# Kernel tuning notes

Measured on AMD Instinct MI355X. Metric: run time of the kernel, lower is better.

The kernel has to match this reference:

```python
import jax, jax.numpy as jnp
import numpy as np

D_MODEL = 2048
N_HEADS = 16
DIM_K = 128
DIM_V = 128
D_MID = 6144
STD = 0.02


def setup_inputs() -> dict:
    key = jax.random.key(0)
    k_x, k_wq, k_wo, k_K, k_V = jax.random.split(key, 5)
    B, T = 2, 2048
    x = jax.random.normal(k_x, (B, T, D_MODEL), dtype=jnp.float32)
    # nn.Linear weights: stored as (out, in); we keep jax convention (in, out)
    Wq = jax.random.normal(k_wq, (D_MODEL, N_HEADS * DIM_K), dtype=jnp.float32) * (1.0 / np.sqrt(D_MODEL))
    Wo = jax.random.normal(k_wo, (N_HEADS * DIM_V, D_MODEL), dtype=jnp.float32) * (1.0 / np.sqrt(N_HEADS * DIM_V))
    K = jax.random.normal(k_K, (N_HEADS, D_MID, DIM_K), dtype=jnp.float32) * STD
    V = jax.random.normal(k_V, (N_HEADS, D_MID, DIM_V), dtype=jnp.float32) * STD
    return {"x": x, "Wq": Wq, "Wo": Wo, "K": K, "V": V}


def reference(x, Wq, Wo, K, V):
    B, T, _ = x.shape
    # Q projection: (b,t,d) @ (d, h*dk) -> (b,t,h,dk)
    Q = (x @ Wq).reshape(B, T, N_HEADS, DIM_K)
    # per-head GEMM 1: (b,t,h,dk) x (h,m,dk) -> (b,t,h,m)
    scores = jnp.einsum('bthk,hmk->bthm', Q, K)
    scores = jax.nn.silu(scores)
    # per-head GEMM 2: (b,t,h,m) x (h,m,dv) -> (b,t,h,dv)
    out = jnp.einsum('bthm,hmv->bthv', scores, V)
    out = out.reshape(B, T, N_HEADS * DIM_V)
    return out @ Wo
```

## Files before the change

kernel.cpp:

```cpp
#include <hip/hip_runtime.h>

typedef unsigned short ushort_t;
typedef __attribute__((ext_vector_type(8))) short bf16x8;
typedef __attribute__((ext_vector_type(4))) float f32x4;
typedef __attribute__((ext_vector_type(4))) unsigned int u32x4;

__device__ __forceinline__ unsigned short f2b(float f) {
  unsigned u = __builtin_bit_cast(unsigned, f);
  u += 0x7fffu + ((u >> 16) & 1u);
  return (unsigned short)(u >> 16);
}

__device__ __forceinline__ float silu_f(float x) {
  float e = __builtin_amdgcn_exp2f(x * -1.44269504f);
  return x * __builtin_amdgcn_rcpf(1.0f + e);
}

__device__ __forceinline__ void silu_pack(const f32x4 s, unsigned& p0, unsigned& p1) {
  float v0 = silu_f(s[0]), v1 = silu_f(s[1]), v2 = silu_f(s[2]), v3 = silu_f(s[3]);
  asm("v_cvt_pk_bf16_f32 %0, %1, %2" : "=v"(p0) : "v"(v0), "v"(v1));
  asm("v_cvt_pk_bf16_f32 %0, %1, %2" : "=v"(p1) : "v"(v2), "v"(v3));
}

__device__ __forceinline__ void gload_lds16(const ushort_t* g, ushort_t* l) {
  auto* gp = (const __attribute__((address_space(1))) ushort_t*)g;
  auto* lp = (__attribute__((address_space(3))) ushort_t*)l;
  __builtin_amdgcn_global_load_lds(gp, lp, 16, 0, 0);
}

__device__ __forceinline__ void storeC(float* C, size_t i, float v) { C[i] = v; }
__device__ __forceinline__ void storeC(ushort_t* C, size_t i, float v) { C[i] = f2b(v); }


__global__ __launch_bounds__(256) void cast_f32_bf16_k(const float4* __restrict__ in,
                                                       ushort4* __restrict__ out, int n4) {
  int i = blockIdx.x * 256 + threadIdx.x;
  if (i < n4) {
    float4 v = in[i];
    ushort4 o;
    o.x = f2b(v.x); o.y = f2b(v.y); o.z = f2b(v.z); o.w = f2b(v.w);
    out[i] = o;
  }
}

__global__ __launch_bounds__(256) void transpose_cast_k(const float* __restrict__ in,
                                                        ushort_t* __restrict__ out,
                                                        int rows, int cols) {
  __shared__ float tile[64][65];
  size_t boff = (size_t)blockIdx.z * rows * cols;
  const float* inb = in + boff;
  ushort_t* outb = out + boff;
  int r0 = blockIdx.y * 64, c0 = blockIdx.x * 64;
  int lr = threadIdx.x >> 6, lc = threadIdx.x & 63;
#pragma unroll
  for (int i = 0; i < 16; i++) {
    int r = i * 4 + lr;
    tile[r][lc] = inb[(size_t)(r0 + r) * cols + (c0 + lc)];
  }
  __syncthreads();
#pragma unroll
  for (int i = 0; i < 16; i++) {
    int oc = i * 4 + lr;
    outb[(size_t)(c0 + oc) * rows + (r0 + lc)] = f2b(tile[lc][oc]);
  }
}


template <typename OutT>
__global__ __launch_bounds__(256) void gemm_bt_k(const ushort_t* __restrict__ A,
                                                 const ushort_t* __restrict__ BT,
                                                 OutT* __restrict__ C, int M, int N, int K) {
  __shared__ alignas(16) ushort_t lA[2][128 * 32];
  __shared__ alignas(16) ushort_t lB[2][128 * 32];
  int tid = threadIdx.x, lane = tid & 63, wave = tid >> 6;
  int wm = wave >> 1, wn = wave & 1;
  int m0 = blockIdx.y * 128, n0 = blockIdx.x * 128;
  int lr = lane & 15, lk = lane >> 4;
  f32x4 acc[4][4] = {};

#define STG(B, K0)                                                                   \
  {                                                                                  \
    _Pragma("unroll") for (int t = 0; t < 2; t++) {                                  \
      int cb = wave * 128 + t * 64;                                                  \
      int c = cb + lane;                                                             \
      int r = c >> 2;                                                                \
      int kc = (c & 3) ^ ((r >> 1) & 3);                                             \
      gload_lds16(A + (size_t)(m0 + r) * K + (K0) + kc * 8, lA[B] + (size_t)cb * 8); \
      gload_lds16(BT + (size_t)(n0 + r) * K + (K0) + kc * 8, lB[B] + (size_t)cb * 8);\
    }                                                                                \
  }

  STG(0, 0);
  int cur = 0;
  for (int k0 = 0; k0 < K; k0 += 32, cur ^= 1) {
    asm volatile("s_waitcnt vmcnt(0)" ::: "memory");
    __builtin_amdgcn_s_barrier();
    asm volatile("" ::: "memory");
    if (k0 + 32 < K) STG(cur ^ 1, k0 + 32);
    bf16x8 aF[4], bF[4];
#pragma unroll
    for (int i = 0; i < 4; i++) {
      int r = wm * 64 + i * 16 + lr;
      int kc = lk ^ ((r >> 1) & 3);
      aF[i] = *(const bf16x8*)(lA[cur] + r * 32 + kc * 8);
    }
#pragma unroll
    for (int j = 0; j < 4; j++) {
      int r = wn * 64 + j * 16 + lr;
      int kc = lk ^ ((r >> 1) & 3);
      bF[j] = *(const bf16x8*)(lB[cur] + r * 32 + kc * 8);
    }
#pragma unroll
    for (int i = 0; i < 4; i++)
#pragma unroll
      for (int j = 0; j < 4; j++)
        acc[i][j] = __builtin_amdgcn_mfma_f32_16x16x32_bf16(aF[i], bF[j], acc[i][j], 0, 0, 0);
  }
#undef STG
#pragma unroll
  for (int i = 0; i < 4; i++) {
#pragma unroll
    for (int j = 0; j < 4; j++) {
      int row = m0 + wm * 64 + i * 16 + lk * 4;
      int col = n0 + wn * 64 + j * 16 + lr;
#pragma unroll
      for (int r = 0; r < 4; r++) storeC(C, (size_t)(row + r) * N + col, acc[i][j][r]);
    }
  }
}


#define MFMA_BF16 __builtin_amdgcn_mfma_f32_16x16x32_bf16

__global__ __launch_bounds__(256) void fused_mid_k(const ushort_t* __restrict__ Qb,
                                                   const ushort_t* __restrict__ Kb,
                                                   const ushort_t* __restrict__ VTb,
                                                   ushort_t* __restrict__ mid) {
  __shared__ alignas(16) ushort_t lK[2][64 * 128];
  __shared__ alignas(16) ushort_t lV[2][128 * 64];
  int tid = threadIdx.x, lane = tid & 63, wave = tid >> 6;
  int lr = lane & 15, lk = lane >> 4;
  int id = blockIdx.x;
  int h = (id & 7) * 2 + (id >> 8);
  int t0 = ((id >> 3) & 31) * 128;
  const ushort_t* Qh = Qb + (size_t)t0 * 2048 + h * 128;
  const ushort_t* Kh = Kb + (size_t)h * 6144 * 128;
  const ushort_t* Vh = VTb + (size_t)h * 128 * 6144;

  bf16x8 qF[2][4];
#pragma unroll
  for (int tj = 0; tj < 2; tj++)
#pragma unroll
    for (int ks = 0; ks < 4; ks++)
      qF[tj][ks] = *(const bf16x8*)(Qh + (size_t)(wave * 32 + tj * 16 + lr) * 2048 + ks * 32 + lk * 8);

#define STAGE(B, M0)                                                              \
  {                                                                               \
    _Pragma("unroll") for (int t = 0; t < 4; t++) {                               \
      int c = (wave * 4 + t) * 64 + lane;                                         \
      int ik = c >> 4;                                                            \
      int pik = (ik & 0x20) | ((ik & 0x0C) << 1) | ((ik & 0x10) >> 2) | (ik & 3); \
      int sk = (c & 15) ^ (ik & 15);                                              \
      gload_lds16(Kh + (size_t)((M0) + pik) * 128 + sk * 8, lK[B] + (size_t)c * 8); \
      int iv = c >> 3;                                                            \
      int sv = (c & 7) ^ (iv & 7);                                                \
      gload_lds16(Vh + (size_t)iv * 6144 + (M0) + sv * 8, lV[B] + (size_t)c * 8); \
    }                                                                             \
  }

  STAGE(0, 0);

  f32x4 acc[2][8] = {};
  int cur = 0;
  for (int m0 = 0; m0 < 6144; m0 += 64, cur ^= 1) {
    asm volatile("s_waitcnt vmcnt(0)" ::: "memory");
    __builtin_amdgcn_s_barrier();
    asm volatile("" ::: "memory");
    if (m0 + 64 < 6144) STAGE(cur ^ 1, m0 + 64);

    __builtin_amdgcn_s_setprio(1);
    f32x4 s2[4][2] = {};
    unsigned P[4][2][2];
#pragma unroll
    for (int ks = 0; ks < 4; ks++) {
      bf16x8 k0 = *(const bf16x8*)(lK[cur] + (0 * 16 + lr) * 128 + (((ks * 4 + lk) ^ lr) * 8));
      bf16x8 k1 = *(const bf16x8*)(lK[cur] + (1 * 16 + lr) * 128 + (((ks * 4 + lk) ^ lr) * 8));
      s2[0][0] = MFMA_BF16(k0, qF[0][ks], s2[0][0], 0, 0, 0);
      s2[0][1] = MFMA_BF16(k0, qF[1][ks], s2[0][1], 0, 0, 0);
      s2[1][0] = MFMA_BF16(k1, qF[0][ks], s2[1][0], 0, 0, 0);
      s2[1][1] = MFMA_BF16(k1, qF[1][ks], s2[1][1], 0, 0, 0);
    }
#pragma unroll
    for (int ks = 0; ks < 4; ks++) {
      bf16x8 k2 = *(const bf16x8*)(lK[cur] + (2 * 16 + lr) * 128 + (((ks * 4 + lk) ^ lr) * 8));
      bf16x8 k3 = *(const bf16x8*)(lK[cur] + (3 * 16 + lr) * 128 + (((ks * 4 + lk) ^ lr) * 8));
      s2[2][0] = MFMA_BF16(k2, qF[0][ks], s2[2][0], 0, 0, 0);
      s2[2][1] = MFMA_BF16(k2, qF[1][ks], s2[2][1], 0, 0, 0);
      s2[3][0] = MFMA_BF16(k3, qF[0][ks], s2[3][0], 0, 0, 0);
      s2[3][1] = MFMA_BF16(k3, qF[1][ks], s2[3][1], 0, 0, 0);
      {
        int mj = ks >> 1, tjj = ks & 1;
        silu_pack(s2[mj][tjj], P[mj][tjj][0], P[mj][tjj][1]);
      }
    }
    bf16x8 aF0[2];
#pragma unroll
    for (int tj = 0; tj < 2; tj++) {
      u32x4 w;
      w.x = P[0][tj][0]; w.y = P[0][tj][1]; w.z = P[1][tj][0]; w.w = P[1][tj][1];
      aF0[tj] = __builtin_bit_cast(bf16x8, w);
    }
#pragma unroll
    for (int vj = 0; vj < 8; vj++) {
      bf16x8 vF = *(const bf16x8*)(lV[cur] + (vj * 16 + lr) * 64 + ((lk ^ (lr & 7)) * 8));
      acc[0][vj] = MFMA_BF16(aF0[0], vF, acc[0][vj], 0, 0, 0);
      acc[1][vj] = MFMA_BF16(aF0[1], vF, acc[1][vj], 0, 0, 0);
      if (vj < 4) {
        int mj = 2 + (vj >> 1), tjj = vj & 1;
        silu_pack(s2[mj][tjj], P[mj][tjj][0], P[mj][tjj][1]);
      }
    }
    bf16x8 aF1[2];
#pragma unroll
    for (int tj = 0; tj < 2; tj++) {
      u32x4 w;
      w.x = P[2][tj][0]; w.y = P[2][tj][1]; w.z = P[3][tj][0]; w.w = P[3][tj][1];
      aF1[tj] = __builtin_bit_cast(bf16x8, w);
    }
#pragma unroll
    for (int vj = 0; vj < 8; vj++) {
      bf16x8 vF = *(const bf16x8*)(lV[cur] + (vj * 16 + lr) * 64 + (((4 + lk) ^ (lr & 7)) * 8));
      acc[0][vj] = MFMA_BF16(aF1[0], vF, acc[0][vj], 0, 0, 0);
      acc[1][vj] = MFMA_BF16(aF1[1], vF, acc[1][vj], 0, 0, 0);
    }
    __builtin_amdgcn_s_setprio(0);
  }
#undef STAGE
#pragma unroll
  for (int tj = 0; tj < 2; tj++) {
#pragma unroll
    for (int vj = 0; vj < 8; vj++) {
      int row = t0 + wave * 32 + tj * 16 + lk * 4;
      int col = h * 128 + vj * 16 + lr;
#pragma unroll
      for (int r = 0; r < 4; r++) mid[(size_t)(row + r) * 2048 + col] = f2b(acc[tj][vj][r]);
    }
  }
}


extern "C" void kernel_launch(void* const* d_in, const int* in_sizes, int n_in,
                              void* d_out, int out_size, void* d_ws, size_t ws_size,
                              hipStream_t stream) {
  const float* x  = (const float*)d_in[0];
  const float* Wq = (const float*)d_in[1];
  const float* Wo = (const float*)d_in[2];
  const float* K  = (const float*)d_in[3];
  const float* V  = (const float*)d_in[4];
  float* out = (float*)d_out;

  ushort_t* xb   = (ushort_t*)d_ws;
  ushort_t* WqT  = xb + 8388608;
  ushort_t* WoT  = WqT + 4194304;
  ushort_t* Kb   = WoT + 4194304;
  ushort_t* VTb  = Kb + 12582912;
  ushort_t* Qb   = VTb + 12582912;
  ushort_t* midb = xb;

  cast_f32_bf16_k<<<8192, 256, 0, stream>>>((const float4*)x, (ushort4*)xb, 2097152);
  cast_f32_bf16_k<<<12288, 256, 0, stream>>>((const float4*)K, (ushort4*)Kb, 3145728);
  transpose_cast_k<<<dim3(32, 32, 1), 256, 0, stream>>>(Wq, WqT, 2048, 2048);
  transpose_cast_k<<<dim3(32, 32, 1), 256, 0, stream>>>(Wo, WoT, 2048, 2048);
  transpose_cast_k<<<dim3(2, 96, 16), 256, 0, stream>>>(V, VTb, 6144, 128);

  gemm_bt_k<ushort_t><<<dim3(16, 32), 256, 0, stream>>>(xb, WqT, Qb, 4096, 2048, 2048);
  fused_mid_k<<<512, 256, 0, stream>>>(Qb, Kb, VTb, midb);
  gemm_bt_k<float><<<dim3(16, 32), 256, 0, stream>>>(midb, WoT, out, 4096, 2048, 2048);
}
```

Before: 363.1 us.

## Double token tile per block in fused mid kernel to reuse K/V tiles

Each block now processes 256 tokens (64 per wave) instead of 128, halving the grid to 256 blocks, which matches the 256 CUs on MI355X. Every staged K/V LDS tile feeds twice as many MFMAs, reducing global and LDS traffic per unit of compute. The cost is much higher register use (doubled accumulators and Q fragments), only one block per CU, and less latency hiding or possible spills.

```diff
diff --git a/kernel.cpp b/kernel.cpp
--- a/kernel.cpp
+++ b/kernel.cpp
@@ -132,27 +132,27 @@
 
 #define MFMA_BF16 __builtin_amdgcn_mfma_f32_16x16x32_bf16
 
-__global__ __launch_bounds__(256) void fused_mid_k(const ushort_t* __restrict__ Qb,
-                                                   const ushort_t* __restrict__ Kb,
-                                                   const ushort_t* __restrict__ VTb,
-                                                   ushort_t* __restrict__ mid) {
+__global__ __launch_bounds__(256, 1) void fused_mid_k(const ushort_t* __restrict__ Qb,
+                                                      const ushort_t* __restrict__ Kb,
+                                                      const ushort_t* __restrict__ VTb,
+                                                      ushort_t* __restrict__ mid) {
   __shared__ alignas(16) ushort_t lK[2][64 * 128];
   __shared__ alignas(16) ushort_t lV[2][128 * 64];
   int tid = threadIdx.x, lane = tid & 63, wave = tid >> 6;
   int lr = lane & 15, lk = lane >> 4;
   int id = blockIdx.x;
-  int h = (id & 7) * 2 + (id >> 8);
-  int t0 = ((id >> 3) & 31) * 128;
+  int h = (id & 7) * 2 + (id >> 7);
+  int t0 = ((id >> 3) & 15) * 256;
   const ushort_t* Qh = Qb + (size_t)t0 * 2048 + h * 128;
   const ushort_t* Kh = Kb + (size_t)h * 6144 * 128;
   const ushort_t* Vh = VTb + (size_t)h * 128 * 6144;
 
-  bf16x8 qF[2][4];
-#pragma unroll
-  for (int tj = 0; tj < 2; tj++)
+  bf16x8 qF[4][4];
+#pragma unroll
+  for (int tj = 0; tj < 4; tj++)
 #pragma unroll
     for (int ks = 0; ks < 4; ks++)
-      qF[tj][ks] = *(const bf16x8*)(Qh + (size_t)(wave * 32 + tj * 16 + lr) * 2048 + ks * 32 + lk * 8);
+      qF[tj][ks] = *(const bf16x8*)(Qh + (size_t)(wave * 64 + tj * 16 + lr) * 2048 + ks * 32 + lk * 8);
 
 #define STAGE(B, M0)                                                              \
   {                                                                               \
@@ -170,7 +170,7 @@
 
   STAGE(0, 0);
 
-  f32x4 acc[2][8] = {};
+  f32x4 acc[4][8] = {};
   int cur = 0;
   for (int m0 = 0; m0 < 6144; m0 += 64, cur ^= 1) {
     asm volatile("s_waitcnt vmcnt(0)" ::: "memory");
@@ -179,68 +179,68 @@
     if (m0 + 64 < 6144) STAGE(cur ^ 1, m0 + 64);
 
     __builtin_amdgcn_s_setprio(1);
-    f32x4 s2[4][2] = {};
-    unsigned P[4][2][2];
+    f32x4 s2a[2][4] = {};
 #pragma unroll
     for (int ks = 0; ks < 4; ks++) {
       bf16x8 k0 = *(const bf16x8*)(lK[cur] + (0 * 16 + lr) * 128 + (((ks * 4 + lk) ^ lr) * 8));
       bf16x8 k1 = *(const bf16x8*)(lK[cur] + (1 * 16 + lr) * 128 + (((ks * 4 + lk) ^ lr) * 8));
-      s2[0][0] = MFMA_BF16(k0, qF[0][ks], s2[0][0], 0, 0, 0);
-      s2[0][1] = MFMA_BF16(k0, qF[1][ks], s2[0][1], 0, 0, 0);
-      s2[1][0] = MFMA_BF16(k1, qF[0][ks], s2[1][0], 0, 0, 0);
-      s2[1][1] = MFMA_BF16(k1, qF[1][ks], s2[1][1], 0, 0, 0);
-    }
+#pragma unroll
+      for (int tj = 0; tj < 4; tj++) {
+        s2a[0][tj] = MFMA_BF16(k0, qF[tj][ks], s2a[0][tj], 0, 0, 0);
+        s2a[1][tj] = MFMA_BF16(k1, qF[tj][ks], s2a[1][tj], 0, 0, 0);
+      }
+    }
+    f32x4 s2b[2][4] = {};
+    unsigned Pa[2][4][2], Pb[2][4][2];
 #pragma unroll
     for (int ks = 0; ks < 4; ks++) {
       bf16x8 k2 = *(const bf16x8*)(lK[cur] + (2 * 16 + lr) * 128 + (((ks * 4 + lk) ^ lr) * 8));
       bf16x8 k3 = *(const bf16x8*)(lK[cur] + (3 * 16 + lr) * 128 + (((ks * 4 + lk) ^ lr) * 8));
-      s2[2][0] = MFMA_BF16(k2, qF[0][ks], s2[2][0], 0, 0, 0);
-      s2[2][1] = MFMA_BF16(k2, qF[1][ks], s2[2][1], 0, 0, 0);
-      s2[3][0] = MFMA_BF16(k3, qF[0][ks], s2[3][0], 0, 0, 0);
-      s2[3][1] = MFMA_BF16(k3, qF[1][ks], s2[3][1], 0, 0, 0);
-      {
-        int mj = ks >> 1, tjj = ks & 1;
-        silu_pack(s2[mj][tjj], P[mj][tjj][0], P[mj][tjj][1]);
+#pragma unroll
+      for (int tj = 0; tj < 4; tj++) {
+        s2b[0][tj] = MFMA_BF16(k2, qF[tj][ks], s2b[0][tj], 0, 0, 0);
+        s2b[1][tj] = MFMA_BF16(k3, qF[tj][ks], s2b[1][tj], 0, 0, 0);
       }
-    }
-    bf16x8 aF0[2];
-#pragma unroll
-    for (int tj = 0; tj < 2; tj++) {
+      silu_pack(s2a[0][ks], Pa[0][ks][0], Pa[0][ks][1]);
+      silu_pack(s2a[1][ks], Pa[1][ks][0], Pa[1][ks][1]);
+    }
+    bf16x8 aF0[4];
+#pragma unroll
+    for (int tj = 0; tj < 4; tj++) {
       u32x4 w;
-      w.x = P[0][tj][0]; w.y = P[0][tj][1]; w.z = P[1][tj][0]; w.w = P[1][tj][1];
+      w.x = Pa[0][tj][0]; w.y = Pa[0][tj][1]; w.z = Pa[1][tj][0]; w.w = Pa[1][tj][1];
       aF0[tj] = __builtin_bit_cast(bf16x8, w);
     }
 #pragma unroll
     for (int vj = 0; vj < 8; vj++) {
       bf16x8 vF = *(const bf16x8*)(lV[cur] + (vj * 16 + lr) * 64 + ((lk ^ (lr & 7)) * 8));
-      acc[0][vj] = MFMA_BF16(aF0[0], vF, acc[0][vj], 0, 0, 0);
-      acc[1][vj] = MFMA_BF16(aF0[1], vF, acc[1][vj], 0, 0, 0);
-      if (vj < 4) {
-        int mj = 2 + (vj >> 1), tjj = vj & 1;
-        silu_pack(s2[mj][tjj], P[mj][tjj][0], P[mj][tjj][1]);
-      }
-    }
-    bf16x8 aF1[2];
-#pragma unroll
-    for (int tj = 0; tj < 2; tj++) {
+#pragma unroll
+      for (int tj = 0; tj < 4; tj++)
+        acc[tj][vj] = MFMA_BF16(aF0[tj], vF, acc[tj][vj], 0, 0, 0);
+      silu_pack(s2b[vj >> 2][vj & 3], Pb[vj >> 2][vj & 3][0], Pb[vj >> 2][vj & 3][1]);
+    }
+    bf16x8 aF1[4];
+#pragma unroll
+    for (int tj = 0; tj < 4; tj++) {
       u32x4 w;
-      w.x = P[2][tj][0]; w.y = P[2][tj][1]; w.z = P[3][tj][0]; w.w = P[3][tj][1];
+      w.x = Pb[0][tj][0]; w.y = Pb[0][tj][1]; w.z = Pb[1][tj][0]; w.w = Pb[1][tj][1];
       aF1[tj] = __builtin_bit_cast(bf16x8, w);
     }
 #pragma unroll
     for (int vj = 0; vj < 8; vj++) {
       bf16x8 vF = *(const bf16x8*)(lV[cur] + (vj * 16 + lr) * 64 + (((4 + lk) ^ (lr & 7)) * 8));
-      acc[0][vj] = MFMA_BF16(aF1[0], vF, acc[0][vj], 0, 0, 0);
-      acc[1][vj] = MFMA_BF16(aF1[1], vF, acc[1][vj], 0, 0, 0);
+#pragma unroll
+      for (int tj = 0; tj < 4; tj++)
+        acc[tj][vj] = MFMA_BF16(aF1[tj], vF, acc[tj][vj], 0, 0, 0);
     }
     __builtin_amdgcn_s_setprio(0);
   }
 #undef STAGE
 #pragma unroll
-  for (int tj = 0; tj < 2; tj++) {
+  for (int tj = 0; tj < 4; tj++) {
 #pragma unroll
     for (int vj = 0; vj < 8; vj++) {
-      int row = t0 + wave * 32 + tj * 16 + lk * 4;
+      int row = t0 + wave * 64 + tj * 16 + lk * 4;
       int col = h * 128 + vj * 16 + lr;
 #pragma unroll
       for (int r = 0; r < 4; r++) mid[(size_t)(row + r) * 2048 + col] = f2b(acc[tj][vj][r]);
@@ -274,6 +274,6 @@
   transpose_cast_k<<<dim3(2, 96, 16), 256, 0, stream>>>(V, VTb, 6144, 128);
 
   gemm_bt_k<ushort_t><<<dim3(16, 32), 256, 0, stream>>>(xb, WqT, Qb, 4096, 2048, 2048);
-  fused_mid_k<<<512, 256, 0, stream>>>(Qb, Kb, VTb, midb);
+  fused_mid_k<<<256, 256, 0, stream>>>(Qb, Kb, VTb, midb);
   gemm_bt_k<float><<<dim3(16, 32), 256, 0, stream>>>(midb, WoT, out, 4096, 2048, 2048);
 }
```

Measured after the change: 460.0 us. +26.7%, slower.
